# Kernel tuning notes

Hardware: AMD Instinct MI355X
Metric: run time of the kernel (lower is better)

The kernel has to match this reference:

```python
import jax, jax.numpy as jnp
import numpy as np

NEG_SLOPE = 0.2  # PyG GATv2Conv default

N_NODES = 10000
N_EDGES = 320000
DIM_IN = 128
DIM_H = 32
HEADS = 8
DIM_OUT = 32
HID = DIM_H * HEADS  # 256


def _gatv2(x, src, dst, Wl, Wr, att, bias, heads, ch, n):
    # x: [N, Fin]; src/dst: [E] (self-loops already included)
    xl = (x @ Wl).reshape(n, heads, ch)  # source-side transform
    xr = (x @ Wr).reshape(n, heads, ch)  # target-side transform
    e = jax.nn.leaky_relu(xl[src] + xr[dst], NEG_SLOPE)       # [E, H, C]
    score = jnp.einsum('ehc,hc->eh', e, att)                  # [E, H]
    m = jax.ops.segment_max(score, dst, num_segments=n)        # [N, H]
    ex = jnp.exp(score - m[dst])
    denom = jax.ops.segment_sum(ex, dst, num_segments=n)
    alpha = ex / (denom[dst] + 1e-16)                          # [E, H]
    out = jax.ops.segment_sum(alpha[:, :, None] * xl[src], dst, num_segments=n)
    return out.reshape(n, heads * ch) + bias


def setup_inputs() -> dict:
    key = jax.random.key(0)
    ks = jax.random.split(key, 16)
    x = jax.random.normal(ks[0], (N_NODES, DIM_IN), dtype=jnp.float32)
    edge_index = jax.random.randint(ks[1], (2, N_EDGES), 0, N_NODES, dtype=jnp.int64)

    def glorot(k, shape, fan_in):
        return jax.random.normal(k, shape, dtype=jnp.float32) * (1.0 / np.sqrt(fan_in))

    return {
        'x': x,
        'W1l': glorot(ks[2], (DIM_IN, HID), DIM_IN),
        'W1r': glorot(ks[3], (DIM_IN, HID), DIM_IN),
        'a1': glorot(ks[4], (HEADS, DIM_H), DIM_H),
        'b1': jnp.zeros((HID,), dtype=jnp.float32),
        'W2l': glorot(ks[5], (HID, HID), HID),
        'W2r': glorot(ks[6], (HID, HID), HID),
        'a2': glorot(ks[7], (HEADS, DIM_H), DIM_H),
        'b2': jnp.zeros((HID,), dtype=jnp.float32),
        'W3l': glorot(ks[8], (HID, DIM_OUT), HID),
        'W3r': glorot(ks[9], (HID, DIM_OUT), HID),
        'a3': glorot(ks[10], (1, DIM_OUT), DIM_OUT),
        'b3': jnp.zeros((DIM_OUT,), dtype=jnp.float32),
        'edge_index': edge_index,
    }


def reference(x, W1l, W1r, a1, b1, W2l, W2r, a2, b2, W3l, W3r, a3, b3, edge_index):
    n = x.shape[0]
    loops = jnp.arange(n, dtype=edge_index.dtype)
    src = jnp.concatenate([edge_index[0], loops])
    dst = jnp.concatenate([edge_index[1], loops])

    # eval mode: dropout(p=0.6) is identity
    h = _gatv2(x, src, dst, W1l, W1r, a1, b1, HEADS, DIM_H, n)
    h = jax.nn.relu(h)
    h_res = h
    h = _gatv2(h, src, dst, W2l, W2r, a2, b2, HEADS, DIM_H, n)
    h = h + h_res
    h = _gatv2(h, src, dst, W3l, W3r, a3, b3, 1, DIM_OUT, n)
    return h
```

## Files before the change

### kernel.cpp

```cpp
#include <hip/hip_runtime.h>

#define N_NODES 10000
#define N_EDGES 320000
#define E_TOT   (N_EDGES + N_NODES)
#define HID 256
#define NEG_SLOPE 0.2f
#define SLOTS 192

typedef __attribute__((ext_vector_type(8))) short short8;
typedef __attribute__((ext_vector_type(4))) float float4v;

__device__ int   g_cnt[N_NODES];
__device__ int   g_csr[(size_t)N_NODES * SLOTS];
__device__ __align__(16) float g_xl[(size_t)N_NODES * HID];
__device__ __align__(16) float g_xr[(size_t)N_NODES * HID];
__device__ __align__(16) float g_h1[(size_t)N_NODES * HID];
__device__ __align__(16) unsigned short g_xlb[(size_t)N_NODES * HID];
__device__ __align__(16) unsigned short g_abf[(size_t)N_NODES * 512];
__device__ __align__(16) unsigned short g_bp1a[16 * 8  * 64 * 8];
__device__ __align__(16) unsigned short g_bp2a[16 * 8  * 64 * 8];
__device__ __align__(16) unsigned short g_bp1b[16 * 16 * 64 * 8];
__device__ __align__(16) unsigned short g_bp2b[16 * 16 * 64 * 8];
__device__ __align__(16) unsigned short g_bp1c[2  * 16 * 64 * 8];
__device__ __align__(16) unsigned short g_bp2c[2  * 16 * 64 * 8];

#define LOG2E 1.44269504088896340736f

__device__ __forceinline__ unsigned short f2bf(float f) {
    unsigned int u = __float_as_uint(f);
    unsigned int r = (u + 0x7fffu + ((u >> 16) & 1u)) >> 16;
    return (unsigned short)r;
}
__device__ __forceinline__ float bf2f(unsigned short h) {
    return __uint_as_float(((unsigned int)h) << 16);
}
__device__ __forceinline__ unsigned int splitpack(float f) {
    unsigned short hi = f2bf(f);
    unsigned short lo = f2bf(f - bf2f(hi));
    return ((unsigned int)lo << 16) | hi;
}

__device__ __forceinline__ void packB(const float* __restrict__ B,
                                      unsigned short* __restrict__ Bp,
                                      int t, int nkc, int N) {
    int lane = t & 63;
    int kc   = (t >> 6) % nkc;
    int nt   = (t >> 6) / nkc;
    int n = nt * 16 + (lane & 15);
    int kbase = kc * 32 + (lane >> 4) * 8;
    #pragma unroll
    for (int j = 0; j < 8; ++j) {
        int kp = kbase + j;
        int k  = kp >> 1;
        float f = B[(size_t)k * N + n];
        unsigned short hi = f2bf(f);
        Bp[(size_t)t * 8 + j] = (kp & 1) ? f2bf(f - bf2f(hi)) : hi;
    }
}

__global__ __launch_bounds__(256) void k_prep(const float* __restrict__ W1l,
                                              const float* __restrict__ W1r,
                                              int* __restrict__ cnt) {
    const int S0 = 16 * 8 * 64;
    int t = blockIdx.x * blockDim.x + threadIdx.x;
    if (t < S0) {
        packB(W1l, g_bp1a, t, 8, 256);
        packB(W1r, g_bp2a, t, 8, 256);
    } else {
        int u = t - S0;
        if (u < N_NODES) cnt[u] = 0;
    }
}

#define FILL_BLOCKS  ((E_TOT + 255) / 256)
#define GEMM1_BLOCKS ((N_NODES + 31) / 32)
#define PACK2_BLOCKS ((16 * 16 * 64 + 2 * 16 * 64 + 255) / 256)
__global__ __launch_bounds__(256) void k_fill_gemm1(
    const int* __restrict__ ei,
    int* __restrict__ cnt, int* __restrict__ csr,
    const float4* __restrict__ A4,
    const short8* __restrict__ Bp1, const short8* __restrict__ Bp2,
    unsigned short* __restrict__ C1b,
    float* __restrict__ C2,
    const float* __restrict__ W2l, const float* __restrict__ W2r,
    const float* __restrict__ W3l, const float* __restrict__ W3r)
{
    if (blockIdx.x < FILL_BLOCKS) {
        int e = blockIdx.x * 256 + threadIdx.x;
        if (e < E_TOT) {
            int src, dst;
            if (e < N_EDGES) { src = ei[e]; dst = ei[N_EDGES + e]; }
            else             { src = dst = e - N_EDGES; }
            int pos = atomicAdd(&cnt[dst], 1);
            if (pos < SLOTS) csr[dst * SLOTS + pos] = src;
        }
        return;
    }
    if (blockIdx.x >= FILL_BLOCKS + GEMM1_BLOCKS) {
        const int S1 = 16 * 16 * 64;
        const int S2 = 2 * 16 * 64;
        int t = (blockIdx.x - FILL_BLOCKS - GEMM1_BLOCKS) * 256 + threadIdx.x;
        if (t < S1) {
            packB(W2l, g_bp1b, t, 16, 256);
            packB(W2r, g_bp2b, t, 16, 256);
        } else {
            int u = t - S1;
            if (u < S2) {
                packB(W3l, g_bp1c, u, 16, 32);
                packB(W3r, g_bp2c, u, 16, 32);
            }
        }
        return;
    }
    const int nkc = 8;
    int mt   = blockIdx.x - FILL_BLOCKS;
    int lane = threadIdx.x & 63;
    int wid  = threadIdx.x >> 6;
    int quad = lane >> 4;
    int col  = lane & 15;
    int r0 = mt * 32 + col;       if (r0 >= N_NODES) r0 = N_NODES - 1;
    int r1 = mt * 32 + 16 + col;  if (r1 >= N_NODES) r1 = N_NODES - 1;
    const float4* a0 = A4 + (size_t)r0 * 32 + quad;
    const float4* a1 = A4 + (size_t)r1 * 32 + quad;
    float4v acc[2][4][2];
    #pragma unroll
    for (int s = 0; s < 2; ++s)
        #pragma unroll
        for (int t = 0; t < 4; ++t) { acc[s][t][0] = (float4v)(0.f); acc[s][t][1] = (float4v)(0.f); }
    for (int kc = 0; kc < nkc; ++kc) {
        float4 v0 = a0[kc * 4];
        float4 v1 = a1[kc * 4];
        union { short8 s; unsigned int u[4]; } c0, c1;
        c0.u[0] = splitpack(v0.x); c0.u[1] = splitpack(v0.y);
        c0.u[2] = splitpack(v0.z); c0.u[3] = splitpack(v0.w);
        c1.u[0] = splitpack(v1.x); c1.u[1] = splitpack(v1.y);
        c1.u[2] = splitpack(v1.z); c1.u[3] = splitpack(v1.w);
        short8 A0 = c0.s, A1 = c1.s;
        #pragma unroll
        for (int t = 0; t < 4; ++t) {
            int nt = wid * 4 + t;
            size_t bi = ((size_t)(nt * nkc + kc)) * 64 + lane;
            short8 b1 = Bp1[bi];
            short8 b2 = Bp2[bi];
            acc[0][t][0] = __builtin_amdgcn_mfma_f32_16x16x32_bf16(A0, b1, acc[0][t][0], 0, 0, 0);
            acc[0][t][1] = __builtin_amdgcn_mfma_f32_16x16x32_bf16(A0, b2, acc[0][t][1], 0, 0, 0);
            acc[1][t][0] = __builtin_amdgcn_mfma_f32_16x16x32_bf16(A1, b1, acc[1][t][0], 0, 0, 0);
            acc[1][t][1] = __builtin_amdgcn_mfma_f32_16x16x32_bf16(A1, b2, acc[1][t][1], 0, 0, 0);
        }
    }
    #pragma unroll
    for (int s = 0; s < 2; ++s) {
        #pragma unroll
        for (int t = 0; t < 4; ++t) {
            int gc = (wid * 4 + t) * 16 + col;
            #pragma unroll
            for (int r = 0; r < 4; ++r) {
                int row = mt * 32 + s * 16 + quad * 4 + r;
                if (row < N_NODES) {
                    C1b[(size_t)row * 256 + gc] = f2bf(acc[s][t][0][r]);
                    C2[(size_t)row * 256 + gc]  = acc[s][t][1][r];
                }
            }
        }
    }
}

__global__ __launch_bounds__(256) void k_mgemm2(const short8* __restrict__ Af,
                                                const short8* __restrict__ Bp1,
                                                const short8* __restrict__ Bp2,
                                                unsigned short* __restrict__ C1b,
                                                float* __restrict__ C2,
                                                int Kp, int nkc) {
    int mt   = blockIdx.x;
    int lane = threadIdx.x & 63;
    int wid  = threadIdx.x >> 6;
    int quad = lane >> 4;
    int col  = lane & 15;
    int ks   = Kp >> 3;
    int r0 = mt * 32 + col;       if (r0 >= N_NODES) r0 = N_NODES - 1;
    int r1 = mt * 32 + 16 + col;  if (r1 >= N_NODES) r1 = N_NODES - 1;
    const short8* a0 = Af + (size_t)r0 * ks + quad;
    const short8* a1 = Af + (size_t)r1 * ks + quad;
    float4v acc[2][4][2];
    #pragma unroll
    for (int s = 0; s < 2; ++s)
        #pragma unroll
        for (int t = 0; t < 4; ++t) { acc[s][t][0] = (float4v)(0.f); acc[s][t][1] = (float4v)(0.f); }
    for (int kc = 0; kc < nkc; ++kc) {
        short8 A0 = a0[kc * 4];
        short8 A1 = a1[kc * 4];
        #pragma unroll
        for (int t = 0; t < 4; ++t) {
            int nt = wid * 4 + t;
            size_t bi = ((size_t)(nt * nkc + kc)) * 64 + lane;
            short8 b1 = Bp1[bi];
            short8 b2 = Bp2[bi];
            acc[0][t][0] = __builtin_amdgcn_mfma_f32_16x16x32_bf16(A0, b1, acc[0][t][0], 0, 0, 0);
            acc[0][t][1] = __builtin_amdgcn_mfma_f32_16x16x32_bf16(A0, b2, acc[0][t][1], 0, 0, 0);
            acc[1][t][0] = __builtin_amdgcn_mfma_f32_16x16x32_bf16(A1, b1, acc[1][t][0], 0, 0, 0);
            acc[1][t][1] = __builtin_amdgcn_mfma_f32_16x16x32_bf16(A1, b2, acc[1][t][1], 0, 0, 0);
        }
    }
    #pragma unroll
    for (int s = 0; s < 2; ++s) {
        #pragma unroll
        for (int t = 0; t < 4; ++t) {
            int gc = (wid * 4 + t) * 16 + col;
            #pragma unroll
            for (int r = 0; r < 4; ++r) {
                int row = mt * 32 + s * 16 + quad * 4 + r;
                if (row < N_NODES) {
                    C1b[(size_t)row * 256 + gc] = f2bf(acc[s][t][0][r]);
                    C2[(size_t)row * 256 + gc]  = acc[s][t][1][r];
                }
            }
        }
    }
}

__global__ __launch_bounds__(256) void k_mgemm32(const short8* __restrict__ Af,
                                                 const short8* __restrict__ Bp1,
                                                 const short8* __restrict__ Bp2,
                                                 float* __restrict__ C1,
                                                 float* __restrict__ C2) {
    int mt   = blockIdx.x;
    int lane = threadIdx.x & 63;
    int wid  = threadIdx.x >> 6;
    int quad = lane >> 4;
    int col  = lane & 15;
    int nt   = wid & 1;
    const short8* Bp = (wid < 2) ? Bp1 : Bp2;
    float* C = (wid < 2) ? C1 : C2;

    const short8* abase = Af + (size_t)(mt * 16 + col) * 64 + quad;
    float4v acc = (float4v)(0.f);
    #pragma unroll 4
    for (int kc = 0; kc < 16; ++kc) {
        short8 a = abase[kc * 4];
        short8 b = Bp[((size_t)(nt * 16 + kc)) * 64 + lane];
        acc = __builtin_amdgcn_mfma_f32_16x16x32_bf16(a, b, acc, 0, 0, 0);
    }
    #pragma unroll
    for (int r = 0; r < 4; ++r)
        C[(size_t)(mt * 16 + quad * 4 + r) * 32 + nt * 16 + col] = acc[r];
}

__global__ __launch_bounds__(256) void k_agg8(const unsigned short* __restrict__ xlb,
                                              const float4* __restrict__ xr4,
                                              const float4* __restrict__ att4,
                                              const float4* __restrict__ bias4,
                                              const int* __restrict__ cnt,
                                              const int* __restrict__ csr_src,
                                              const float4* __restrict__ res4,
                                              float4* __restrict__ out4,
                                              uint4* __restrict__ abf_out,
                                              int mode) {
    int node = blockIdx.x * 4 + (threadIdx.x >> 6);
    if (node >= N_NODES) return;
    int lane = threadIdx.x & 63;
    float4 xrv = xr4[(size_t)node * 64 + lane];
    float4 av  = att4[lane];
    av.x *= LOG2E; av.y *= LOG2E; av.z *= LOG2E; av.w *= LOG2E;
    int c = cnt[node]; if (c > SLOTS) c = SLOTS;
    int base0 = node * SLOTS;

    float s = 0.f;
    float4 acc = make_float4(0.f, 0.f, 0.f, 0.f);

    for (int base = 0; base < c; base += 64) {
        int li = base + lane;
        int idxv = csr_src[base0 + (li < c ? li : c - 1)];
        int m = c - base; if (m > 64) m = 64;
        for (int j0 = 0; j0 < m; j0 += 8) {
            int srcs[8];
            ushort4 uv[8];
            #pragma unroll
            for (int j = 0; j < 8; ++j)
                srcs[j] = __shfl(idxv, j0 + j);
            #pragma unroll
            for (int j = 0; j < 8; ++j)
                uv[j] = *(const ushort4*)(xlb + (size_t)srcs[j] * 256 + 4 * lane);
            #pragma unroll
            for (int j = 0; j < 8; ++j) {
                if (j0 + j < m) {
                    float4 xv;
                    xv.x = bf2f(uv[j].x); xv.y = bf2f(uv[j].y);
                    xv.z = bf2f(uv[j].z); xv.w = bf2f(uv[j].w);
                    float tx = xv.x + xrv.x, ty = xv.y + xrv.y;
                    float tz = xv.z + xrv.z, tw = xv.w + xrv.w;
                    float w = fmaxf(tx, NEG_SLOPE * tx) * av.x
                            + fmaxf(ty, NEG_SLOPE * ty) * av.y
                            + fmaxf(tz, NEG_SLOPE * tz) * av.z
                            + fmaxf(tw, NEG_SLOPE * tw) * av.w;
                    w += __shfl_xor(w, 1);
                    w += __shfl_xor(w, 2);
                    w += __shfl_xor(w, 4);
                    float p = exp2f(w);
                    s += p;
                    acc.x += p * xv.x;
                    acc.y += p * xv.y;
                    acc.z += p * xv.z;
                    acc.w += p * xv.w;
                }
            }
        }
    }

    float inv = 1.f / (s + 1e-16f);
    float4 bv = bias4[lane];
    float4 o;
    o.x = acc.x * inv + bv.x; o.y = acc.y * inv + bv.y;
    o.z = acc.z * inv + bv.z; o.w = acc.w * inv + bv.w;
    if (mode == 0) {
        o.x = fmaxf(o.x, 0.f); o.y = fmaxf(o.y, 0.f);
        o.z = fmaxf(o.z, 0.f); o.w = fmaxf(o.w, 0.f);
    } else {
        float4 r = res4[(size_t)node * 64 + lane];
        o.x += r.x; o.y += r.y; o.z += r.z; o.w += r.w;
    }
    if (out4) out4[(size_t)node * 64 + lane] = o;
    if (abf_out) {
        uint4 u;
        u.x = splitpack(o.x); u.y = splitpack(o.y);
        u.z = splitpack(o.z); u.w = splitpack(o.w);
        abf_out[(size_t)node * 64 + lane] = u;
    }
}

__global__ __launch_bounds__(256) void k_agg1(const float4* __restrict__ xl4,
                                              const float4* __restrict__ xr4,
                                              const float4* __restrict__ att4,
                                              const float4* __restrict__ bias4,
                                              const int* __restrict__ cnt,
                                              const int* __restrict__ csr_src,
                                              float4* __restrict__ out4) {
    int node = blockIdx.x * 4 + (threadIdx.x >> 6);
    if (node >= N_NODES) return;
    int lane = threadIdx.x & 63;
    int q = lane & 7;
    int grp = lane >> 3;
    float4 xrv = xr4[(size_t)node * 8 + q];
    float4 av  = att4[q];
    av.x *= LOG2E; av.y *= LOG2E; av.z *= LOG2E; av.w *= LOG2E;
    int c = cnt[node]; if (c > SLOTS) c = SLOTS;
    int start = node * SLOTS, end = start + c;
    float s = 0.f;
    float4 acc = make_float4(0.f, 0.f, 0.f, 0.f);
    for (int i = start + grp; i < end; i += 16) {
        int i2 = i + 8;
        bool has2 = i2 < end;
        int src0 = csr_src[i];
        int src1 = csr_src[has2 ? i2 : i];
        float4 xv0 = xl4[(size_t)src0 * 8 + q];
        float4 xv1 = xl4[(size_t)src1 * 8 + q];
        {
            float tx = xv0.x + xrv.x, ty = xv0.y + xrv.y;
            float tz = xv0.z + xrv.z, tw = xv0.w + xrv.w;
            float w = fmaxf(tx, NEG_SLOPE * tx) * av.x
                    + fmaxf(ty, NEG_SLOPE * ty) * av.y
                    + fmaxf(tz, NEG_SLOPE * tz) * av.z
                    + fmaxf(tw, NEG_SLOPE * tw) * av.w;
            w += __shfl_xor(w, 1);
            w += __shfl_xor(w, 2);
            w += __shfl_xor(w, 4);
            float p = exp2f(w);
            s += p;
            acc.x += p * xv0.x;
            acc.y += p * xv0.y;
            acc.z += p * xv0.z;
            acc.w += p * xv0.w;
        }
        if (has2) {
            float tx = xv1.x + xrv.x, ty = xv1.y + xrv.y;
            float tz = xv1.z + xrv.z, tw = xv1.w + xrv.w;
            float w = fmaxf(tx, NEG_SLOPE * tx) * av.x
                    + fmaxf(ty, NEG_SLOPE * ty) * av.y
                    + fmaxf(tz, NEG_SLOPE * tz) * av.z
                    + fmaxf(tw, NEG_SLOPE * tw) * av.w;
            w += __shfl_xor(w, 1);
            w += __shfl_xor(w, 2);
            w += __shfl_xor(w, 4);
            float p = exp2f(w);
            s += p;
            acc.x += p * xv1.x;
            acc.y += p * xv1.y;
            acc.z += p * xv1.z;
            acc.w += p * xv1.w;
        }
    }
    #pragma unroll
    for (int off = 8; off < 64; off <<= 1) {
        s     += __shfl_xor(s, off);
        acc.x += __shfl_xor(acc.x, off);
        acc.y += __shfl_xor(acc.y, off);
        acc.z += __shfl_xor(acc.z, off);
        acc.w += __shfl_xor(acc.w, off);
    }
    if (grp == 0) {
        float inv = 1.f / (s + 1e-16f);
        float4 bv = bias4[q];
        float4 o;
        o.x = acc.x * inv + bv.x; o.y = acc.y * inv + bv.y;
        o.z = acc.z * inv + bv.z; o.w = acc.w * inv + bv.w;
        out4[(size_t)node * 8 + q] = o;
    }
}


extern "C" void kernel_launch(void* const* d_in, const int* in_sizes, int n_in,
                              void* d_out, int out_size, void* d_ws, size_t ws_size,
                              hipStream_t stream) {
    const float* x   = (const float*)d_in[0];
    const float* W1l = (const float*)d_in[1];
    const float* W1r = (const float*)d_in[2];
    const float* a1  = (const float*)d_in[3];
    const float* b1  = (const float*)d_in[4];
    const float* W2l = (const float*)d_in[5];
    const float* W2r = (const float*)d_in[6];
    const float* a2  = (const float*)d_in[7];
    const float* b2  = (const float*)d_in[8];
    const float* W3l = (const float*)d_in[9];
    const float* W3r = (const float*)d_in[10];
    const float* a3  = (const float*)d_in[11];
    const float* b3  = (const float*)d_in[12];
    const int*   ei  = (const int*)d_in[13];
    float* out = (float*)d_out;

    int *cnt, *csr;
    float *xl, *xr, *h1;
    unsigned short *xlb, *abf, *bp1a, *bp2a, *bp1b, *bp2b, *bp1c, *bp2c;
    hipGetSymbolAddress((void**)&cnt,    HIP_SYMBOL(g_cnt));
    hipGetSymbolAddress((void**)&csr,    HIP_SYMBOL(g_csr));
    hipGetSymbolAddress((void**)&xl,     HIP_SYMBOL(g_xl));
    hipGetSymbolAddress((void**)&xr,     HIP_SYMBOL(g_xr));
    hipGetSymbolAddress((void**)&h1,     HIP_SYMBOL(g_h1));
    hipGetSymbolAddress((void**)&xlb,    HIP_SYMBOL(g_xlb));
    hipGetSymbolAddress((void**)&abf,    HIP_SYMBOL(g_abf));
    hipGetSymbolAddress((void**)&bp1a,   HIP_SYMBOL(g_bp1a));
    hipGetSymbolAddress((void**)&bp2a,   HIP_SYMBOL(g_bp2a));
    hipGetSymbolAddress((void**)&bp1b,   HIP_SYMBOL(g_bp1b));
    hipGetSymbolAddress((void**)&bp2b,   HIP_SYMBOL(g_bp2b));
    hipGetSymbolAddress((void**)&bp1c,   HIP_SYMBOL(g_bp1c));
    hipGetSymbolAddress((void**)&bp2c,   HIP_SYMBOL(g_bp2c));

    k_prep<<<(16 * 8 * 64 + N_NODES + 255) / 256, 256, 0, stream>>>(W1l, W1r, cnt);

    k_fill_gemm1<<<FILL_BLOCKS + GEMM1_BLOCKS + PACK2_BLOCKS, 256, 0, stream>>>(
        ei, cnt, csr, (const float4*)x,
        (const short8*)bp1a, (const short8*)bp2a, xlb, xr,
        W2l, W2r, W3l, W3r);

    k_agg8<<<(N_NODES + 3) / 4, 256, 0, stream>>>(xlb, (const float4*)xr,
                                        (const float4*)a1, (const float4*)b1,
                                        cnt, csr, nullptr, (float4*)h1,
                                        (uint4*)abf, 0);

    k_mgemm2<<<(N_NODES + 31) / 32, 256, 0, stream>>>((const short8*)abf,
                                                      (const short8*)bp1b, (const short8*)bp2b,
                                                      xlb, xr, 512, 16);

    k_agg8<<<(N_NODES + 3) / 4, 256, 0, stream>>>(xlb, (const float4*)xr,
                                        (const float4*)a2, (const float4*)b2,
                                        cnt, csr, (const float4*)h1, nullptr,
                                        (uint4*)abf, 1);

    k_mgemm32<<<N_NODES / 16, 256, 0, stream>>>((const short8*)abf,
                                                (const short8*)bp1c, (const short8*)bp2c,
                                                xl, xr);

    k_agg1<<<(N_NODES + 3) / 4, 256, 0, stream>>>((const float4*)xl, (const float4*)xr,
                                                  (const float4*)a3, (const float4*)b3,
                                                  cnt, csr, (float4*)out);
}
```

Baseline: 228.3 us.

## Split 8-head aggregation into two half-feature passes using global symbols directly

Each 8-head aggregation kernel is replaced by two templated launches, each covering half of the 256 features. Within a pass, the wave's two 32-lane halves process alternate edges and combine their partial sums with a cross-half shuffle. The aim is a smaller per-pass gather working set (128 bf16 columns of xl) for better cache hit rates, and more independent gathers in flight. Kernels now reference global device symbols directly instead of taking pointer arguments, which removes several hipGetSymbolAddress calls. The cost is extra launches, and the xr and csr reads plus the softmax work are repeated in both passes.

```diff
diff --git a/kernel.cpp b/kernel.cpp
--- a/kernel.cpp
+++ b/kernel.cpp
@@ -79,9 +79,6 @@
     const int* __restrict__ ei,
     int* __restrict__ cnt, int* __restrict__ csr,
     const float4* __restrict__ A4,
-    const short8* __restrict__ Bp1, const short8* __restrict__ Bp2,
-    unsigned short* __restrict__ C1b,
-    float* __restrict__ C2,
     const float* __restrict__ W2l, const float* __restrict__ W2r,
     const float* __restrict__ W3l, const float* __restrict__ W3r)
 {
@@ -118,6 +115,8 @@
     int wid  = threadIdx.x >> 6;
     int quad = lane >> 4;
     int col  = lane & 15;
+    const short8* Bp1 = (const short8*)g_bp1a;
+    const short8* Bp2 = (const short8*)g_bp2a;
     int r0 = mt * 32 + col;       if (r0 >= N_NODES) r0 = N_NODES - 1;
     int r1 = mt * 32 + 16 + col;  if (r1 >= N_NODES) r1 = N_NODES - 1;
     const float4* a0 = A4 + (size_t)r0 * 32 + quad;
@@ -157,30 +156,28 @@
             for (int r = 0; r < 4; ++r) {
                 int row = mt * 32 + s * 16 + quad * 4 + r;
                 if (row < N_NODES) {
-                    C1b[(size_t)row * 256 + gc] = f2bf(acc[s][t][0][r]);
-                    C2[(size_t)row * 256 + gc]  = acc[s][t][1][r];
+                    g_xlb[(size_t)row * 256 + gc] = f2bf(acc[s][t][0][r]);
+                    g_xr [(size_t)row * 256 + gc] = acc[s][t][1][r];
                 }
             }
         }
     }
 }
 
-__global__ __launch_bounds__(256) void k_mgemm2(const short8* __restrict__ Af,
-                                                const short8* __restrict__ Bp1,
-                                                const short8* __restrict__ Bp2,
-                                                unsigned short* __restrict__ C1b,
-                                                float* __restrict__ C2,
-                                                int Kp, int nkc) {
+__global__ __launch_bounds__(256) void k_mgemm2() {
+    const int nkc = 16;
     int mt   = blockIdx.x;
     int lane = threadIdx.x & 63;
     int wid  = threadIdx.x >> 6;
     int quad = lane >> 4;
     int col  = lane & 15;
-    int ks   = Kp >> 3;
+    const short8* Af  = (const short8*)g_abf;
+    const short8* Bp1 = (const short8*)g_bp1b;
+    const short8* Bp2 = (const short8*)g_bp2b;
     int r0 = mt * 32 + col;       if (r0 >= N_NODES) r0 = N_NODES - 1;
     int r1 = mt * 32 + 16 + col;  if (r1 >= N_NODES) r1 = N_NODES - 1;
-    const short8* a0 = Af + (size_t)r0 * ks + quad;
-    const short8* a1 = Af + (size_t)r1 * ks + quad;
+    const short8* a0 = Af + (size_t)r0 * 64 + quad;
+    const short8* a1 = Af + (size_t)r1 * 64 + quad;
     float4v acc[2][4][2];
     #pragma unroll
     for (int s = 0; s < 2; ++s)
@@ -210,29 +207,25 @@
             for (int r = 0; r < 4; ++r) {
                 int row = mt * 32 + s * 16 + quad * 4 + r;
                 if (row < N_NODES) {
-                    C1b[(size_t)row * 256 + gc] = f2bf(acc[s][t][0][r]);
-                    C2[(size_t)row * 256 + gc]  = acc[s][t][1][r];
+                    g_xlb[(size_t)row * 256 + gc] = f2bf(acc[s][t][0][r]);
+                    g_xr [(size_t)row * 256 + gc] = acc[s][t][1][r];
                 }
             }
         }
     }
 }
 
-__global__ __launch_bounds__(256) void k_mgemm32(const short8* __restrict__ Af,
-                                                 const short8* __restrict__ Bp1,
-                                                 const short8* __restrict__ Bp2,
-                                                 float* __restrict__ C1,
-                                                 float* __restrict__ C2) {
+__global__ __launch_bounds__(256) void k_mgemm32() {
     int mt   = blockIdx.x;
     int lane = threadIdx.x & 63;
     int wid  = threadIdx.x >> 6;
     int quad = lane >> 4;
     int col  = lane & 15;
     int nt   = wid & 1;
-    const short8* Bp = (wid < 2) ? Bp1 : Bp2;
-    float* C = (wid < 2) ? C1 : C2;
-
-    const short8* abase = Af + (size_t)(mt * 16 + col) * 64 + quad;
+    const short8* Bp = (wid < 2) ? (const short8*)g_bp1c : (const short8*)g_bp2c;
+    float* C = (wid < 2) ? g_xl : g_xr;
+
+    const short8* abase = (const short8*)g_abf + (size_t)(mt * 16 + col) * 64 + quad;
     float4v acc = (float4v)(0.f);
     #pragma unroll 4
     for (int kc = 0; kc < 16; ++kc) {
@@ -245,23 +238,18 @@
         C[(size_t)(mt * 16 + quad * 4 + r) * 32 + nt * 16 + col] = acc[r];
 }
 
-__global__ __launch_bounds__(256) void k_agg8(const unsigned short* __restrict__ xlb,
-                                              const float4* __restrict__ xr4,
-                                              const float4* __restrict__ att4,
-                                              const float4* __restrict__ bias4,
-                                              const int* __restrict__ cnt,
-                                              const int* __restrict__ csr_src,
-                                              const float4* __restrict__ res4,
-                                              float4* __restrict__ out4,
-                                              uint4* __restrict__ abf_out,
-                                              int mode) {
+template<int MODE, int PASS>
+__global__ __launch_bounds__(256) void k_agg8h(const float4* __restrict__ att4,
+                                               const float4* __restrict__ bias4) {
     int node = blockIdx.x * 4 + (threadIdx.x >> 6);
     if (node >= N_NODES) return;
     int lane = threadIdx.x & 63;
-    float4 xrv = xr4[(size_t)node * 64 + lane];
-    float4 av  = att4[lane];
+    int hl   = lane & 31;
+    int half = lane >> 5;
+    float4 xrv = ((const float4*)g_xr)[(size_t)node * 64 + PASS * 32 + hl];
+    float4 av  = att4[PASS * 32 + hl];
     av.x *= LOG2E; av.y *= LOG2E; av.z *= LOG2E; av.w *= LOG2E;
-    int c = cnt[node]; if (c > SLOTS) c = SLOTS;
+    int c = g_cnt[node]; if (c > SLOTS) c = SLOTS;
     int base0 = node * SLOTS;
 
     float s = 0.f;
@@ -269,23 +257,23 @@
 
     for (int base = 0; base < c; base += 64) {
         int li = base + lane;
-        int idxv = csr_src[base0 + (li < c ? li : c - 1)];
+        int idxv = g_csr[base0 + (li < c ? li : c - 1)];
         int m = c - base; if (m > 64) m = 64;
         for (int j0 = 0; j0 < m; j0 += 8) {
-            int srcs[8];
-            ushort4 uv[8];
+            int srcs[4];
+            ushort4 uv[4];
             #pragma unroll
-            for (int j = 0; j < 8; ++j)
-                srcs[j] = __shfl(idxv, j0 + j);
+            for (int k = 0; k < 4; ++k)
+                srcs[k] = __shfl(idxv, j0 + 2 * k + half);
             #pragma unroll
-            for (int j = 0; j < 8; ++j)
-                uv[j] = *(const ushort4*)(xlb + (size_t)srcs[j] * 256 + 4 * lane);
+            for (int k = 0; k < 4; ++k)
+                uv[k] = *(const ushort4*)(g_xlb + (size_t)srcs[k] * 256 + PASS * 128 + 4 * hl);
             #pragma unroll
-            for (int j = 0; j < 8; ++j) {
-                if (j0 + j < m) {
+            for (int k = 0; k < 4; ++k) {
+                if (j0 + 2 * k + half < m) {
                     float4 xv;
-                    xv.x = bf2f(uv[j].x); xv.y = bf2f(uv[j].y);
-                    xv.z = bf2f(uv[j].z); xv.w = bf2f(uv[j].w);
+                    xv.x = bf2f(uv[k].x); xv.y = bf2f(uv[k].y);
+                    xv.z = bf2f(uv[k].z); xv.w = bf2f(uv[k].w);
                     float tx = xv.x + xrv.x, ty = xv.y + xrv.y;
                     float tz = xv.z + xrv.z, tw = xv.w + xrv.w;
                     float w = fmaxf(tx, NEG_SLOPE * tx) * av.x
@@ -306,51 +294,56 @@
         }
     }
 
+    s += __shfl_xor(s, 32);
+    acc.x += __shfl_xor(acc.x, 32);
+    acc.y += __shfl_xor(acc.y, 32);
+    acc.z += __shfl_xor(acc.z, 32);
+    acc.w += __shfl_xor(acc.w, 32);
+
     float inv = 1.f / (s + 1e-16f);
-    float4 bv = bias4[lane];
+    float4 bv = bias4[PASS * 32 + hl];
     float4 o;
     o.x = acc.x * inv + bv.x; o.y = acc.y * inv + bv.y;
     o.z = acc.z * inv + bv.z; o.w = acc.w * inv + bv.w;
-    if (mode == 0) {
+    if (MODE == 0) {
         o.x = fmaxf(o.x, 0.f); o.y = fmaxf(o.y, 0.f);
         o.z = fmaxf(o.z, 0.f); o.w = fmaxf(o.w, 0.f);
     } else {
-        float4 r = res4[(size_t)node * 64 + lane];
+        float4 r = ((const float4*)g_h1)[(size_t)node * 64 + PASS * 32 + hl];
         o.x += r.x; o.y += r.y; o.z += r.z; o.w += r.w;
     }
-    if (out4) out4[(size_t)node * 64 + lane] = o;
-    if (abf_out) {
+    if (half == 0) {
+        if (MODE == 0)
+            ((float4*)g_h1)[(size_t)node * 64 + PASS * 32 + hl] = o;
         uint4 u;
         u.x = splitpack(o.x); u.y = splitpack(o.y);
         u.z = splitpack(o.z); u.w = splitpack(o.w);
-        abf_out[(size_t)node * 64 + lane] = u;
-    }
-}
-
-__global__ __launch_bounds__(256) void k_agg1(const float4* __restrict__ xl4,
-                                              const float4* __restrict__ xr4,
-                                              const float4* __restrict__ att4,
+        ((uint4*)g_abf)[(size_t)node * 64 + PASS * 32 + hl] = u;
+    }
+}
+
+__global__ __launch_bounds__(256) void k_agg1(const float4* __restrict__ att4,
                                               const float4* __restrict__ bias4,
-                                              const int* __restrict__ cnt,
-                                              const int* __restrict__ csr_src,
                                               float4* __restrict__ out4) {
     int node = blockIdx.x * 4 + (threadIdx.x >> 6);
     if (node >= N_NODES) return;
     int lane = threadIdx.x & 63;
     int q = lane & 7;
     int grp = lane >> 3;
+    const float4* xl4 = (const float4*)g_xl;
+    const float4* xr4 = (const float4*)g_xr;
     float4 xrv = xr4[(size_t)node * 8 + q];
     float4 av  = att4[q];
     av.x *= LOG2E; av.y *= LOG2E; av.z *= LOG2E; av.w *= LOG2E;
-    int c = cnt[node]; if (c > SLOTS) c = SLOTS;
+    int c = g_cnt[node]; if (c > SLOTS) c = SLOTS;
     int start = node * SLOTS, end = start + c;
     float s = 0.f;
     float4 acc = make_float4(0.f, 0.f, 0.f, 0.f);
     for (int i = start + grp; i < end; i += 16) {
         int i2 = i + 8;
         bool has2 = i2 < end;
-        int src0 = csr_src[i];
-        int src1 = csr_src[has2 ? i2 : i];
+        int src0 = g_csr[i];
+        int src1 = g_csr[has2 ? i2 : i];
         float4 xv0 = xl4[(size_t)src0 * 8 + q];
         float4 xv1 = xl4[(size_t)src1 * 8 + q];
         {
@@ -365,10 +358,8 @@
             w += __shfl_xor(w, 4);
             float p = exp2f(w);
             s += p;
-            acc.x += p * xv0.x;
-            acc.y += p * xv0.y;
-            acc.z += p * xv0.z;
-            acc.w += p * xv0.w;
+            acc.x += p * xv0.x; acc.y += p * xv0.y;
+            acc.z += p * xv0.z; acc.w += p * xv0.w;
         }
         if (has2) {
             float tx = xv1.x + xrv.x, ty = xv1.y + xrv.y;
@@ -382,10 +373,8 @@
             w += __shfl_xor(w, 4);
             float p = exp2f(w);
             s += p;
-            acc.x += p * xv1.x;
-            acc.y += p * xv1.y;
-            acc.z += p * xv1.z;
-            acc.w += p * xv1.w;
+            acc.x += p * xv1.x; acc.y += p * xv1.y;
+            acc.z += p * xv1.z; acc.w += p * xv1.w;
         }
     }
     #pragma unroll
@@ -410,65 +399,42 @@
 extern "C" void kernel_launch(void* const* d_in, const int* in_sizes, int n_in,
                               void* d_out, int out_size, void* d_ws, size_t ws_size,
                               hipStream_t stream) {
-    const float* x   = (const float*)d_in[0];
+    const float4* x4 = (const float4*)d_in[0];
     const float* W1l = (const float*)d_in[1];
     const float* W1r = (const float*)d_in[2];
-    const float* a1  = (const float*)d_in[3];
-    const float* b1  = (const float*)d_in[4];
+    const float4* a1 = (const float4*)d_in[3];
+    const float4* b1 = (const float4*)d_in[4];
     const float* W2l = (const float*)d_in[5];
     const float* W2r = (const float*)d_in[6];
-    const float* a2  = (const float*)d_in[7];
-    const float* b2  = (const float*)d_in[8];
+    const float4* a2 = (const float4*)d_in[7];
+    const float4* b2 = (const float4*)d_in[8];
     const float* W3l = (const float*)d_in[9];
     const float* W3r = (const float*)d_in[10];
-    const float* a3  = (const float*)d_in[11];
-    const float* b3  = (const float*)d_in[12];
+    const float4* a3 = (const float4*)d_in[11];
+    const float4* b3 = (const float4*)d_in[12];
     const int*   ei  = (const int*)d_in[13];
-    float* out = (float*)d_out;
-
-    int *cnt, *csr;
-    float *xl, *xr, *h1;
-    unsigned short *xlb, *abf, *bp1a, *bp2a, *bp1b, *bp2b, *bp1c, *bp2c;
-    hipGetSymbolAddress((void**)&cnt,    HIP_SYMBOL(g_cnt));
-    hipGetSymbolAddress((void**)&csr,    HIP_SYMBOL(g_csr));
-    hipGetSymbolAddress((void**)&xl,     HIP_SYMBOL(g_xl));
-    hipGetSymbolAddress((void**)&xr,     HIP_SYMBOL(g_xr));
-    hipGetSymbolAddress((void**)&h1,     HIP_SYMBOL(g_h1));
-    hipGetSymbolAddress((void**)&xlb,    HIP_SYMBOL(g_xlb));
-    hipGetSymbolAddress((void**)&abf,    HIP_SYMBOL(g_abf));
-    hipGetSymbolAddress((void**)&bp1a,   HIP_SYMBOL(g_bp1a));
-    hipGetSymbolAddress((void**)&bp2a,   HIP_SYMBOL(g_bp2a));
-    hipGetSymbolAddress((void**)&bp1b,   HIP_SYMBOL(g_bp1b));
-    hipGetSymbolAddress((void**)&bp2b,   HIP_SYMBOL(g_bp2b));
-    hipGetSymbolAddress((void**)&bp1c,   HIP_SYMBOL(g_bp1c));
-    hipGetSymbolAddress((void**)&bp2c,   HIP_SYMBOL(g_bp2c));
+    float4* out = (float4*)d_out;
+
+    int* cnt; int* csr;
+    hipGetSymbolAddress((void**)&cnt, HIP_SYMBOL(g_cnt));
+    hipGetSymbolAddress((void**)&csr, HIP_SYMBOL(g_csr));
+
+    const int AGG_BLOCKS = (N_NODES + 3) / 4;
 
     k_prep<<<(16 * 8 * 64 + N_NODES + 255) / 256, 256, 0, stream>>>(W1l, W1r, cnt);
 
     k_fill_gemm1<<<FILL_BLOCKS + GEMM1_BLOCKS + PACK2_BLOCKS, 256, 0, stream>>>(
-        ei, cnt, csr, (const float4*)x,
-        (const short8*)bp1a, (const short8*)bp2a, xlb, xr,
-        W2l, W2r, W3l, W3r);
-
-    k_agg8<<<(N_NODES + 3) / 4, 256, 0, stream>>>(xlb, (const float4*)xr,
-                                        (const float4*)a1, (const float4*)b1,
-                                        cnt, csr, nullptr, (float4*)h1,
-                                        (uint4*)abf, 0);
-
-    k_mgemm2<<<(N_NODES + 31) / 32, 256, 0, stream>>>((const short8*)abf,
-                                                      (const short8*)bp1b, (const short8*)bp2b,
-                                                      xlb, xr, 512, 16);
-
-    k_agg8<<<(N_NODES + 3) / 4, 256, 0, stream>>>(xlb, (const float4*)xr,
-                                        (const float4*)a2, (const float4*)b2,
-                                        cnt, csr, (const float4*)h1, nullptr,
-                                        (uint4*)abf, 1);
-
-    k_mgemm32<<<N_NODES / 16, 256, 0, stream>>>((const short8*)abf,
-                                                (const short8*)bp1c, (const short8*)bp2c,
-                                                xl, xr);
-
-    k_agg1<<<(N_NODES + 3) / 4, 256, 0, stream>>>((const float4*)xl, (const float4*)xr,
-                                                  (const float4*)a3, (const float4*)b3,
-                                                  cnt, csr, (float4*)out);
-}
+        ei, cnt, csr, x4, W2l, W2r, W3l, W3r);
+
+    k_agg8h<0, 0><<<AGG_BLOCKS, 256, 0, stream>>>(a1, b1);
+    k_agg8h<0, 1><<<AGG_BLOCKS, 256, 0, stream>>>(a1, b1);
+
+    k_mgemm2<<<GEMM1_BLOCKS, 256, 0, stream>>>();
+
+    k_agg8h<1, 0><<<AGG_BLOCKS, 256, 0, stream>>>(a2, b2);
+    k_agg8h<1, 1><<<AGG_BLOCKS, 256, 0, stream>>>(a2, b2);
+
+    k_mgemm32<<<N_NODES / 16, 256, 0, stream>>>();
+
+    k_agg1<<<AGG_BLOCKS, 256, 0, stream>>>(a3, b3, out);
+}
```

New measurement: 241.9 us. 6.0% more time.
